# Kernel tuning notes

Measured on AMD Instinct MI355X. Metric: run time of the kernel, lower is better.

Reference implementation:

```python
import jax, jax.numpy as jnp
import numpy as np

N_NODES = 100
F_IN = 65536
C_OUT = 60
ACTION_DIM = 100
N_EDGES = 2000


def setup_inputs() -> dict:
    key = jax.random.key(0)
    ks = jax.random.split(key, 16)
    s = 0.02
    return {
        "substrate_features": jax.random.normal(ks[0], (1, N_NODES, F_IN), jnp.float32),
        "edge_index": jax.random.randint(ks[1], (2, N_EDGES), 0, N_NODES, dtype=jnp.int32),
        "v_cpu_demand_t": jax.random.uniform(ks[2], (1,), jnp.float32),
        "v_bw_demand_t": jax.random.uniform(ks[3], (1,), jnp.float32),
        "num_pending_v_nodes_t": jax.random.uniform(ks[4], (1,), jnp.float32),
        "actor_w": jax.random.normal(ks[5], (3, F_IN, C_OUT), jnp.float32) * s,
        "actor_b": jax.random.normal(ks[6], (C_OUT,), jnp.float32) * s,
        "critic_w": jax.random.normal(ks[7], (3, F_IN, C_OUT), jnp.float32) * s,
        "critic_b": jax.random.normal(ks[8], (C_OUT,), jnp.float32) * s,
        "actor_fc_w": jax.random.normal(ks[9], (N_NODES * C_OUT + 3, ACTION_DIM), jnp.float32) * s,
        "actor_fc_b": jax.random.normal(ks[10], (ACTION_DIM,), jnp.float32) * s,
        "critic_fc_w": jax.random.normal(ks[11], (N_NODES * C_OUT + 3, 1), jnp.float32) * s,
        "critic_fc_b": jax.random.normal(ks[12], (1,), jnp.float32) * s,
    }


def cheb_conv(x, edge_index, W, b):
    # ChebConv, K=3, sym normalization, lambda_max=2 (PyG defaults).
    # With lambda_max=2 the scaled Laplacian is L_hat = -D^{-1/2} A D^{-1/2}
    # (diagonal becomes 0 after the -1 self-loop shift).
    # x: [1, N, F]; edge_index: [2, E]; W: [3, F, C]; b: [C]
    src, dst = edge_index[0], edge_index[1]
    n = x.shape[1]
    deg = jax.ops.segment_sum(jnp.ones(src.shape[0], x.dtype), src, num_segments=n)
    dis = jnp.where(deg > 0, jax.lax.rsqrt(jnp.where(deg > 0, deg, 1.0)), 0.0)
    norm = -(dis[src] * dis[dst])  # [E], L_hat off-diagonal entries
    x2 = x[0]  # [N, F]

    def prop(z):  # z: [N, F] -> L_hat @ z via gather/scatter over edges
        return jax.ops.segment_sum(z[src] * norm[:, None], dst, num_segments=n)

    Tx0 = x2
    Tx1 = prop(Tx0)
    Tx2 = 2.0 * prop(Tx1) - Tx0
    out = Tx0 @ W[0] + Tx1 @ W[1] + Tx2 @ W[2] + b  # [N, C]
    return out[None]  # [1, N, C]


def reference(substrate_features, edge_index, v_cpu_demand_t, v_bw_demand_t,
              num_pending_v_nodes_t, actor_w, actor_b, critic_w, critic_b,
              actor_fc_w, actor_fc_b, critic_fc_w, critic_fc_b):
    emb_a = jnp.tanh(cheb_conv(substrate_features, edge_index, actor_w, actor_b))
    emb_a = emb_a.reshape(1, -1)  # [1, N*60]
    emb_c = jnp.tanh(cheb_conv(substrate_features, edge_index, critic_w, critic_b))
    emb_c = emb_c.reshape(1, -1)
    extras = [v_cpu_demand_t[None], v_bw_demand_t[None], num_pending_v_nodes_t[None]]  # each [1,1]
    state_a = jnp.concatenate([emb_a] + extras, axis=1)  # [1, 6003]
    state_c = jnp.concatenate([emb_c] + extras, axis=1)
    logits = state_a @ actor_fc_w + actor_fc_b  # [1, action_dim]
    values = state_c @ critic_fc_w + critic_fc_b  # [1, 1]
    return (logits, values)
```

## Files before the change

kernel.cpp:

```cpp
#include <hip/hip_runtime.h>
#include <stdint.h>

#define F_IN 65536
#define NN 100
#define CO 60
#define G2 256
#define KC (F_IN/G2)
#define BK 64
#define NIT (KC/BK)
#define AST 72
#define BTILE (BK*CO)
#define BQ3 (3*BTILE/4)

typedef short v8s __attribute__((ext_vector_type(8)));
typedef float v4f __attribute__((ext_vector_type(4)));

__device__ __forceinline__ unsigned int f2bf(float x){
  unsigned int u = __float_as_uint(x);
  u += 0x7fffu + ((u>>16)&1u);
  return u>>16;
}

__device__ __forceinline__ v4f mfma16(v8s a, v8s b, v4f c){
  return __builtin_amdgcn_mfma_f32_16x16x32_bf16(a,b,c,0,0,0);
}

__global__ __launch_bounds__(256,2)
void k_gemm(const float* __restrict__ x, const float* __restrict__ aw,
            const float* __restrict__ cw, float* __restrict__ dst, int partial){
  const int bid  = blockIdx.x;
  const int xcd  = bid & 7, slot = bid >> 3;
  const int net  = slot & 1;
  const int s    = xcd*32 + (slot >> 1);
  const int k0   = s*KC;
  const int tid  = threadIdx.x;
  const int wave = tid>>6, lane = tid&63, quad = lane>>4, nl = lane&15;
  const int c0   = wave*16;
  const int ccl  = min(c0+nl, CO-1);

  const float* Wn = net ? cw : aw;

  __shared__ __align__(16) unsigned short Al[2][112*AST];
  __shared__ __align__(16) unsigned short Bl[2][3*BTILE];

  unsigned int boff[12];
  #pragma unroll
  for(int p=0;p<12;++p){
    int li = min(p*256 + tid, BQ3-1);
    int gp = li/960, fp = li - gp*960;
    boff[p] = (unsigned int)((size_t)gp*F_IN*CO + (size_t)fp*4)*4u;
  }
  const char* bbase0 = (const char*)(Wn + (size_t)k0*CO);

  float4 ra[7];
  float4 rbv[12];
  #pragma unroll
  for(int p=0;p<7;++p){
    int lin = p*256 + tid, row = lin>>4, q = lin&15;
    int rcl = min(row, NN-1);
    ra[p] = *(const float4*)(x + (size_t)rcl*F_IN + k0 + q*4);
  }
  #pragma unroll
  for(int p=0;p<12;++p) rbv[p] = *(const float4*)(bbase0 + boff[p]);

  v4f acc[3][7];
  #pragma unroll
  for(int g=0;g<3;++g)
    #pragma unroll
    for(int i=0;i<7;++i){ v4f z={0.f,0.f,0.f,0.f}; acc[g][i]=z; }

  for(int it=0; it<NIT; ++it){
    unsigned short* buf  = Al[it&1];
    unsigned short* bbuf = Bl[it&1];
    #pragma unroll
    for(int p=0;p<7;++p){
      int lin = p*256 + tid, row = lin>>4, q = lin&15;
      uint2 w;
      w.x = f2bf(ra[p].x) | (f2bf(ra[p].y)<<16);
      w.y = f2bf(ra[p].z) | (f2bf(ra[p].w)<<16);
      *(uint2*)(buf + row*AST + q*4) = w;
    }
    #pragma unroll
    for(int p=0;p<12;++p){
      int lin = p*256 + tid;
      if(lin < BQ3){
        uint2 w;
        w.x = f2bf(rbv[p].x) | (f2bf(rbv[p].y)<<16);
        w.y = f2bf(rbv[p].z) | (f2bf(rbv[p].w)<<16);
        *(uint2*)(bbuf + lin*4) = w;
      }
    }
    __syncthreads();
    if(it+1 < NIT){
      const int kb = k0 + (it+1)*BK;
      #pragma unroll
      for(int p=0;p<7;++p){
        int lin = p*256 + tid, row = lin>>4, q = lin&15;
        int rcl = min(row, NN-1);
        ra[p] = *(const float4*)(x + (size_t)rcl*F_IN + kb + q*4);
      }
      const char* bb2 = bbase0 + (size_t)(it+1)*BK*CO*4;
      #pragma unroll
      for(int p=0;p<12;++p) rbv[p] = *(const float4*)(bb2 + boff[p]);
    }
    v8s fB0[3], fB1[3];
    #pragma unroll
    for(int g=0;g<3;++g){
      const unsigned short* bb = bbuf + g*BTILE + quad*8*CO + ccl;
      #pragma unroll
      for(int j=0;j<8;++j){
        fB0[g][j] = (short)bb[j*CO];
        fB1[g][j] = (short)bb[32*CO + j*CO];
      }
    }
    #pragma unroll
    for(int mt=0; mt<7; ++mt){
      const unsigned short* arow = buf + (mt*16+nl)*AST + quad*8;
      v8s a0 = *(const v8s*)(arow);
      v8s a1 = *(const v8s*)(arow+32);
      #pragma unroll
      for(int g=0;g<3;++g){
        acc[g][mt] = mfma16(a0, fB0[g], acc[g][mt]);
        acc[g][mt] = mfma16(a1, fB1[g], acc[g][mt]);
      }
    }
  }

  const int c = c0 + nl;
  if(c < CO){
    #pragma unroll
    for(int g=0;g<3;++g){
      if(partial){
        float* pd = dst + ((size_t)(net*3+g)*G2 + s)*(NN*CO);
        #pragma unroll
        for(int mt=0;mt<7;++mt){
          #pragma unroll
          for(int i=0;i<4;++i){
            int m = mt*16 + quad*4 + i;
            if(m < NN) pd[m*CO + c] = acc[g][mt][i];
          }
        }
      } else {
        float* pd = dst + (size_t)(net*3+g)*(NN*CO);
        #pragma unroll
        for(int mt=0;mt<7;++mt){
          #pragma unroll
          for(int i=0;i<4;++i){
            int m = mt*16 + quad*4 + i;
            if(m < NN) atomicAdd(pd + m*CO + c, acc[g][mt][i]);
          }
        }
      }
    }
  }
}

__global__ void k_reduce(const float* __restrict__ P, float* __restrict__ Y){
  int o = blockIdx.x*256 + threadIdx.x;
  if(o >= 6*NN*CO) return;
  int gg = o/(NN*CO), r = o - gg*(NN*CO);
  const float* p = P + (size_t)gg*G2*(NN*CO) + (size_t)blockIdx.y*32*(NN*CO) + r;
  float a0=0.f,a1=0.f,a2=0.f,a3=0.f;
  #pragma unroll 2
  for(int s4=0;s4<32;s4+=4){
    a0 += p[(size_t)(s4  )*(NN*CO)];
    a1 += p[(size_t)(s4+1)*(NN*CO)];
    a2 += p[(size_t)(s4+2)*(NN*CO)];
    a3 += p[(size_t)(s4+3)*(NN*CO)];
  }
  atomicAdd(&Y[o], (a0+a1)+(a2+a3));
}

__global__ void k_cheb(const float* __restrict__ Y, const int* __restrict__ ei,
                       const float* __restrict__ ab, const float* __restrict__ cb,
                       float* __restrict__ emb, float* __restrict__ out){
  const int net = blockIdx.x / CO;
  const int c   = blockIdx.x % CO;
  const int t   = threadIdx.x;
  __shared__ float L[NN][NN+1];
  __shared__ float dis[NN];
  __shared__ int   deg[NN];
  __shared__ float y0[NN], y1[NN], y2[NN], zu[NN];

  if(blockIdx.x==0 && t<101) out[t] = 0.f;

  for(int i=t;i<NN*(NN+1);i+=128) ((float*)L)[i]=0.f;
  if(t<NN) deg[t]=0;
  __syncthreads();
  for(int e=t;e<2000;e+=128) atomicAdd(&deg[ei[e]],1);
  __syncthreads();
  if(t<NN) dis[t] = deg[t]>0 ? rsqrtf((float)deg[t]) : 0.f;
  __syncthreads();
  for(int e=t;e<2000;e+=128){
    int s = ei[e], d = ei[2000+e];
    atomicAdd(&L[d][s], -dis[s]*dis[d]);
  }
  if(t<NN){
    const float* yb = Y + (size_t)net*3*NN*CO + t*CO + c;
    y0[t]=yb[0]; y1[t]=yb[NN*CO]; y2[t]=yb[2*NN*CO];
  }
  __syncthreads();
  if(t<NN){
    float s=0.f;
    #pragma unroll 4
    for(int j=0;j<NN;++j) s += L[t][j]*y2[j];
    zu[t] = y1[t] + 2.f*s;
  }
  __syncthreads();
  if(t<NN){
    float s=0.f;
    #pragma unroll 4
    for(int j=0;j<NN;++j) s += L[t][j]*zu[j];
    float b = (net==0) ? ab[c] : cb[c];
    emb[net*NN*CO + t*CO + c] = tanhf(y0[t] - y2[t] + s + b);
  }
}

#define FCB 50
__global__ void k_fc(const float* __restrict__ emb, const float* __restrict__ afw,
                     const float* __restrict__ afb, const float* __restrict__ cfw,
                     const float* __restrict__ cfb, const float* __restrict__ s0,
                     const float* __restrict__ s1, const float* __restrict__ s2,
                     float* __restrict__ out){
  const int b = blockIdx.x;
  const int t = threadIdx.x;
  if(b < FCB){
    const int jj = t & 127, half = t >> 7;
    if(jj < 100){
      const int i0 = b*120 + half*60;
      const float* w = afw + (size_t)i0*100 + jj;
      const float* e = emb + i0;
      float p0=0.f,p1=0.f,p2=0.f,p3=0.f;
      #pragma unroll 3
      for(int i=0;i<60;i+=4){
        p0 += e[i  ]*w[(size_t)(i  )*100];
        p1 += e[i+1]*w[(size_t)(i+1)*100];
        p2 += e[i+2]*w[(size_t)(i+2)*100];
        p3 += e[i+3]*w[(size_t)(i+3)*100];
      }
      atomicAdd(&out[jj], (p0+p1)+(p2+p3));
    }
  } else {
    float p = 0.f;
    const float* e = emb + 6000;
    for(int i=t;i<6000;i+=256) p += e[i]*cfw[i];
    #pragma unroll
    for(int o=32;o>0;o>>=1) p += __shfl_down(p,o,64);
    __shared__ float red[4];
    if((t&63)==0) red[t>>6]=p;
    __syncthreads();
    if(t==0){
      float tot = red[0]+red[1]+red[2]+red[3];
      out[100] = tot + s0[0]*cfw[6000] + s1[0]*cfw[6001] + s2[0]*cfw[6002] + cfb[0];
    }
    if(t<100){
      atomicAdd(&out[t], afb[t] + s0[0]*afw[600000+t] + s1[0]*afw[600100+t] + s2[0]*afw[600200+t]);
    }
  }
}

extern "C" void kernel_launch(void* const* d_in, const int* in_sizes, int n_in,
                              void* d_out, int out_size, void* d_ws, size_t ws_size,
                              hipStream_t stream){
  const float* x   = (const float*)d_in[0];
  const int*   ei  = (const int*)d_in[1];
  const float* s0  = (const float*)d_in[2];
  const float* s1  = (const float*)d_in[3];
  const float* s2  = (const float*)d_in[4];
  const float* aw  = (const float*)d_in[5];
  const float* ab  = (const float*)d_in[6];
  const float* cw  = (const float*)d_in[7];
  const float* cb  = (const float*)d_in[8];
  const float* afw = (const float*)d_in[9];
  const float* afb = (const float*)d_in[10];
  const float* cfw = (const float*)d_in[11];
  const float* cfb = (const float*)d_in[12];
  float* out = (float*)d_out;

  float* Y   = (float*)d_ws;
  float* emb = Y + 6*NN*CO;
  float* P   = emb + 2*NN*CO;
  const size_t need = (size_t)(6*NN*CO + 2*NN*CO + (size_t)6*G2*NN*CO)*sizeof(float);
  const int partial = (ws_size >= need) ? 1 : 0;

  hipMemsetAsync(Y, 0, 6*NN*CO*sizeof(float), stream);

  if(partial){
    k_gemm<<<dim3(512), 256, 0, stream>>>(x, aw, cw, P, 1);
    k_reduce<<<dim3((6*NN*CO+255)/256, 8), 256, 0, stream>>>(P, Y);
  } else {
    k_gemm<<<dim3(512), 256, 0, stream>>>(x, aw, cw, Y, 0);
  }
  k_cheb<<<120, 128, 0, stream>>>(Y, ei, ab, cb, emb, out);
  k_fc<<<FCB+1, 256, 0, stream>>>(emb, afw, afb, cfw, cfb, s0, s1, s2, out);
}
```

Before: 209.1 us.

## Fuse reduce, Chebyshev and FC stages into one grid-barrier kernel; widen GEMM blocks

The split-K reduce, the Chebyshev propagation and the FC heads are merged into a single persistent kernel of 241 blocks. Its stages are separated by software grid barriers on an atomic counter, replacing three launches and the memset of Y. The GEMM block grows from 256 to 512 threads, and the two groups of four waves each take part of the M tiles, which lowers per-thread accumulator registers. The grid barrier assumes all 241 blocks are co-resident, and the reduce now makes a single pass over the 256 partials per output.

```diff
diff --git a/kernel.cpp b/kernel.cpp
--- a/kernel.cpp
+++ b/kernel.cpp
@@ -11,6 +11,7 @@
 #define AST 72
 #define BTILE (BK*CO)
 #define BQ3 (3*BTILE/4)
+#define NB 241
 
 typedef short v8s __attribute__((ext_vector_type(8)));
 typedef float v4f __attribute__((ext_vector_type(4)));
@@ -25,7 +26,7 @@
   return __builtin_amdgcn_mfma_f32_16x16x32_bf16(a,b,c,0,0,0);
 }
 
-__global__ __launch_bounds__(256,2)
+__global__ __launch_bounds__(512,4)
 void k_gemm(const float* __restrict__ x, const float* __restrict__ aw,
             const float* __restrict__ cw, float* __restrict__ dst, int partial){
   const int bid  = blockIdx.x;
@@ -35,7 +36,8 @@
   const int k0   = s*KC;
   const int tid  = threadIdx.x;
   const int wave = tid>>6, lane = tid&63, quad = lane>>4, nl = lane&15;
-  const int c0   = wave*16;
+  const int mh   = wave>>2;
+  const int c0   = (wave&3)*16;
   const int ccl  = min(c0+nl, CO-1);
 
   const float* Wn = net ? cw : aw;
@@ -43,46 +45,47 @@
   __shared__ __align__(16) unsigned short Al[2][112*AST];
   __shared__ __align__(16) unsigned short Bl[2][3*BTILE];
 
-  unsigned int boff[12];
+  const char* bbase0 = (const char*)(Wn + (size_t)k0*CO);
+
+  float4 ra[4];
+  float4 rbv[6];
   #pragma unroll
-  for(int p=0;p<12;++p){
-    int li = min(p*256 + tid, BQ3-1);
-    int gp = li/960, fp = li - gp*960;
-    boff[p] = (unsigned int)((size_t)gp*F_IN*CO + (size_t)fp*4)*4u;
-  }
-  const char* bbase0 = (const char*)(Wn + (size_t)k0*CO);
-
-  float4 ra[7];
-  float4 rbv[12];
-  #pragma unroll
-  for(int p=0;p<7;++p){
-    int lin = p*256 + tid, row = lin>>4, q = lin&15;
+  for(int p=0;p<4;++p){
+    int l2 = min(p*512 + tid, 1791);
+    int row = l2>>4, q = l2&15;
     int rcl = min(row, NN-1);
     ra[p] = *(const float4*)(x + (size_t)rcl*F_IN + k0 + q*4);
   }
   #pragma unroll
-  for(int p=0;p<12;++p) rbv[p] = *(const float4*)(bbase0 + boff[p]);
-
-  v4f acc[3][7];
+  for(int p=0;p<6;++p){
+    int li = min(p*512 + tid, BQ3-1);
+    int gp = li/960, fp = li - gp*960;
+    rbv[p] = *(const float4*)(bbase0 + ((size_t)gp*F_IN*CO + (size_t)fp*4)*4u);
+  }
+
+  v4f acc[3][4];
   #pragma unroll
   for(int g=0;g<3;++g)
     #pragma unroll
-    for(int i=0;i<7;++i){ v4f z={0.f,0.f,0.f,0.f}; acc[g][i]=z; }
+    for(int i=0;i<4;++i){ v4f z={0.f,0.f,0.f,0.f}; acc[g][i]=z; }
 
   for(int it=0; it<NIT; ++it){
     unsigned short* buf  = Al[it&1];
     unsigned short* bbuf = Bl[it&1];
     #pragma unroll
-    for(int p=0;p<7;++p){
-      int lin = p*256 + tid, row = lin>>4, q = lin&15;
-      uint2 w;
-      w.x = f2bf(ra[p].x) | (f2bf(ra[p].y)<<16);
-      w.y = f2bf(ra[p].z) | (f2bf(ra[p].w)<<16);
-      *(uint2*)(buf + row*AST + q*4) = w;
-    }
-    #pragma unroll
-    for(int p=0;p<12;++p){
-      int lin = p*256 + tid;
+    for(int p=0;p<4;++p){
+      int lin = p*512 + tid;
+      if(lin < 1792){
+        int row = lin>>4, q = lin&15;
+        uint2 w;
+        w.x = f2bf(ra[p].x) | (f2bf(ra[p].y)<<16);
+        w.y = f2bf(ra[p].z) | (f2bf(ra[p].w)<<16);
+        *(uint2*)(buf + row*AST + q*4) = w;
+      }
+    }
+    #pragma unroll
+    for(int p=0;p<6;++p){
+      int lin = p*512 + tid;
       if(lin < BQ3){
         uint2 w;
         w.x = f2bf(rbv[p].x) | (f2bf(rbv[p].y)<<16);
@@ -94,14 +97,19 @@
     if(it+1 < NIT){
       const int kb = k0 + (it+1)*BK;
       #pragma unroll
-      for(int p=0;p<7;++p){
-        int lin = p*256 + tid, row = lin>>4, q = lin&15;
+      for(int p=0;p<4;++p){
+        int l2 = min(p*512 + tid, 1791);
+        int row = l2>>4, q = l2&15;
         int rcl = min(row, NN-1);
         ra[p] = *(const float4*)(x + (size_t)rcl*F_IN + kb + q*4);
       }
       const char* bb2 = bbase0 + (size_t)(it+1)*BK*CO*4;
       #pragma unroll
-      for(int p=0;p<12;++p) rbv[p] = *(const float4*)(bb2 + boff[p]);
+      for(int p=0;p<6;++p){
+        int li = min(p*512 + tid, BQ3-1);
+        int gp = li/960, fp = li - gp*960;
+        rbv[p] = *(const float4*)(bb2 + ((size_t)gp*F_IN*CO + (size_t)fp*4)*4u);
+      }
     }
     v8s fB0[3], fB1[3];
     #pragma unroll
@@ -113,41 +121,61 @@
         fB1[g][j] = (short)bb[32*CO + j*CO];
       }
     }
-    #pragma unroll
-    for(int mt=0; mt<7; ++mt){
-      const unsigned short* arow = buf + (mt*16+nl)*AST + quad*8;
-      v8s a0 = *(const v8s*)(arow);
-      v8s a1 = *(const v8s*)(arow+32);
-      #pragma unroll
-      for(int g=0;g<3;++g){
-        acc[g][mt] = mfma16(a0, fB0[g], acc[g][mt]);
-        acc[g][mt] = mfma16(a1, fB1[g], acc[g][mt]);
+    if(mh==0){
+      #pragma unroll
+      for(int m=0;m<4;++m){
+        const unsigned short* arow = buf + (m*16+nl)*AST + quad*8;
+        v8s a0 = *(const v8s*)(arow);
+        v8s a1 = *(const v8s*)(arow+32);
+        #pragma unroll
+        for(int g=0;g<3;++g){
+          acc[g][m] = mfma16(a0, fB0[g], acc[g][m]);
+          acc[g][m] = mfma16(a1, fB1[g], acc[g][m]);
+        }
+      }
+    } else {
+      #pragma unroll
+      for(int m=0;m<3;++m){
+        const unsigned short* arow = buf + ((m+4)*16+nl)*AST + quad*8;
+        v8s a0 = *(const v8s*)(arow);
+        v8s a1 = *(const v8s*)(arow+32);
+        #pragma unroll
+        for(int g=0;g<3;++g){
+          acc[g][m] = mfma16(a0, fB0[g], acc[g][m]);
+          acc[g][m] = mfma16(a1, fB1[g], acc[g][m]);
+        }
       }
     }
   }
 
   const int c = c0 + nl;
+  const int mtb = mh*4;
+  const int mtn = mh ? 3 : 4;
   if(c < CO){
     #pragma unroll
     for(int g=0;g<3;++g){
       if(partial){
         float* pd = dst + ((size_t)(net*3+g)*G2 + s)*(NN*CO);
         #pragma unroll
-        for(int mt=0;mt<7;++mt){
-          #pragma unroll
-          for(int i=0;i<4;++i){
-            int m = mt*16 + quad*4 + i;
-            if(m < NN) pd[m*CO + c] = acc[g][mt][i];
+        for(int m=0;m<4;++m){
+          if(m < mtn){
+            #pragma unroll
+            for(int i=0;i<4;++i){
+              int mm = (mtb+m)*16 + quad*4 + i;
+              if(mm < NN) pd[mm*CO + c] = acc[g][m][i];
+            }
           }
         }
       } else {
         float* pd = dst + (size_t)(net*3+g)*(NN*CO);
         #pragma unroll
-        for(int mt=0;mt<7;++mt){
-          #pragma unroll
-          for(int i=0;i<4;++i){
-            int m = mt*16 + quad*4 + i;
-            if(m < NN) atomicAdd(pd + m*CO + c, acc[g][mt][i]);
+        for(int m=0;m<4;++m){
+          if(m < mtn){
+            #pragma unroll
+            for(int i=0;i<4;++i){
+              int mm = (mtb+m)*16 + quad*4 + i;
+              if(mm < NN) atomicAdd(pd + mm*CO + c, acc[g][m][i]);
+            }
           }
         }
       }
@@ -155,90 +183,98 @@
   }
 }
 
-__global__ void k_reduce(const float* __restrict__ P, float* __restrict__ Y){
-  int o = blockIdx.x*256 + threadIdx.x;
-  if(o >= 6*NN*CO) return;
-  int gg = o/(NN*CO), r = o - gg*(NN*CO);
-  const float* p = P + (size_t)gg*G2*(NN*CO) + (size_t)blockIdx.y*32*(NN*CO) + r;
-  float a0=0.f,a1=0.f,a2=0.f,a3=0.f;
-  #pragma unroll 2
-  for(int s4=0;s4<32;s4+=4){
-    a0 += p[(size_t)(s4  )*(NN*CO)];
-    a1 += p[(size_t)(s4+1)*(NN*CO)];
-    a2 += p[(size_t)(s4+2)*(NN*CO)];
-    a3 += p[(size_t)(s4+3)*(NN*CO)];
-  }
-  atomicAdd(&Y[o], (a0+a1)+(a2+a3));
-}
-
-__global__ void k_cheb(const float* __restrict__ Y, const int* __restrict__ ei,
-                       const float* __restrict__ ab, const float* __restrict__ cb,
-                       float* __restrict__ emb, float* __restrict__ out){
-  const int net = blockIdx.x / CO;
-  const int c   = blockIdx.x % CO;
+__device__ __forceinline__ void gridbar(unsigned* cnt, unsigned target){
+  __syncthreads();
+  if(threadIdx.x==0){
+    __hip_atomic_fetch_add(cnt, 1u, __ATOMIC_ACQ_REL, __HIP_MEMORY_SCOPE_AGENT);
+    while(__hip_atomic_load(cnt, __ATOMIC_ACQUIRE, __HIP_MEMORY_SCOPE_AGENT) < target){}
+  }
+  __syncthreads();
+}
+
+__global__ __launch_bounds__(256,1)
+void k_tail(const float* __restrict__ P, float* __restrict__ Y,
+            const int* __restrict__ ei, const float* __restrict__ ab,
+            const float* __restrict__ cb, const float* __restrict__ afw,
+            const float* __restrict__ afb, const float* __restrict__ cfw,
+            const float* __restrict__ cfb, const float* __restrict__ s0,
+            const float* __restrict__ s1, const float* __restrict__ s2,
+            float* __restrict__ emb, float* __restrict__ out,
+            unsigned* __restrict__ bar, int partial){
+  const int bid = blockIdx.x;
   const int t   = threadIdx.x;
+
   __shared__ float L[NN][NN+1];
   __shared__ float dis[NN];
   __shared__ int   deg[NN];
   __shared__ float y0[NN], y1[NN], y2[NN], zu[NN];
-
-  if(blockIdx.x==0 && t<101) out[t] = 0.f;
-
-  for(int i=t;i<NN*(NN+1);i+=128) ((float*)L)[i]=0.f;
-  if(t<NN) deg[t]=0;
-  __syncthreads();
-  for(int e=t;e<2000;e+=128) atomicAdd(&deg[ei[e]],1);
-  __syncthreads();
-  if(t<NN) dis[t] = deg[t]>0 ? rsqrtf((float)deg[t]) : 0.f;
-  __syncthreads();
-  for(int e=t;e<2000;e+=128){
-    int s = ei[e], d = ei[2000+e];
-    atomicAdd(&L[d][s], -dis[s]*dis[d]);
-  }
-  if(t<NN){
-    const float* yb = Y + (size_t)net*3*NN*CO + t*CO + c;
-    y0[t]=yb[0]; y1[t]=yb[NN*CO]; y2[t]=yb[2*NN*CO];
-  }
-  __syncthreads();
-  if(t<NN){
-    float s=0.f;
-    #pragma unroll 4
-    for(int j=0;j<NN;++j) s += L[t][j]*y2[j];
-    zu[t] = y1[t] + 2.f*s;
-  }
-  __syncthreads();
-  if(t<NN){
-    float s=0.f;
-    #pragma unroll 4
-    for(int j=0;j<NN;++j) s += L[t][j]*zu[j];
-    float b = (net==0) ? ab[c] : cb[c];
-    emb[net*NN*CO + t*CO + c] = tanhf(y0[t] - y2[t] + s + b);
-  }
-}
-
-#define FCB 50
-__global__ void k_fc(const float* __restrict__ emb, const float* __restrict__ afw,
-                     const float* __restrict__ afb, const float* __restrict__ cfw,
-                     const float* __restrict__ cfb, const float* __restrict__ s0,
-                     const float* __restrict__ s1, const float* __restrict__ s2,
-                     float* __restrict__ out){
-  const int b = blockIdx.x;
-  const int t = threadIdx.x;
-  if(b < FCB){
-    const int jj = t & 127, half = t >> 7;
-    if(jj < 100){
-      const int i0 = b*120 + half*60;
-      const float* w = afw + (size_t)i0*100 + jj;
-      const float* e = emb + i0;
-      float p0=0.f,p1=0.f,p2=0.f,p3=0.f;
-      #pragma unroll 3
-      for(int i=0;i<60;i+=4){
-        p0 += e[i  ]*w[(size_t)(i  )*100];
-        p1 += e[i+1]*w[(size_t)(i+1)*100];
-        p2 += e[i+2]*w[(size_t)(i+2)*100];
-        p3 += e[i+3]*w[(size_t)(i+3)*100];
-      }
-      atomicAdd(&out[jj], (p0+p1)+(p2+p3));
+  __shared__ float red[4];
+
+  if(partial){
+    int o = bid*256 + t;
+    if(o < 6*NN*CO){
+      int gg = o/(NN*CO), r = o - gg*(NN*CO);
+      const float* p = P + (size_t)gg*G2*(NN*CO) + r;
+      float a0=0.f,a1=0.f,a2=0.f,a3=0.f;
+      #pragma unroll 4
+      for(int s4=0;s4<G2;s4+=4){
+        a0 += p[(size_t)(s4  )*(NN*CO)];
+        a1 += p[(size_t)(s4+1)*(NN*CO)];
+        a2 += p[(size_t)(s4+2)*(NN*CO)];
+        a3 += p[(size_t)(s4+3)*(NN*CO)];
+      }
+      Y[o] = (a0+a1)+(a2+a3);
+    }
+  }
+  if(bid==130 && t<101) out[t] = 0.f;
+
+  gridbar(bar, NB);
+
+  if(bid < 120){
+    const int net = bid / CO;
+    const int c   = bid % CO;
+    for(int i=t;i<NN*(NN+1);i+=256) ((float*)L)[i]=0.f;
+    if(t<NN) deg[t]=0;
+    __syncthreads();
+    for(int e=t;e<2000;e+=256) atomicAdd(&deg[ei[e]],1);
+    __syncthreads();
+    if(t<NN) dis[t] = deg[t]>0 ? rsqrtf((float)deg[t]) : 0.f;
+    __syncthreads();
+    for(int e=t;e<2000;e+=256){
+      int ss = ei[e], d = ei[2000+e];
+      atomicAdd(&L[d][ss], -dis[ss]*dis[d]);
+    }
+    if(t<NN){
+      const float* yb = Y + (size_t)net*3*NN*CO + t*CO + c;
+      y0[t]=yb[0]; y1[t]=yb[NN*CO]; y2[t]=yb[2*NN*CO];
+    }
+    __syncthreads();
+    if(t<NN){
+      float sv=0.f;
+      #pragma unroll 4
+      for(int j=0;j<NN;++j) sv += L[t][j]*y2[j];
+      zu[t] = y1[t] + 2.f*sv;
+    }
+    __syncthreads();
+    if(t<NN){
+      float sv=0.f;
+      #pragma unroll 4
+      for(int j=0;j<NN;++j) sv += L[t][j]*zu[j];
+      float b = (net==0) ? ab[c] : cb[c];
+      emb[net*NN*CO + t*CO + c] = tanhf(y0[t] - y2[t] + sv + b);
+    }
+  }
+
+  gridbar(bar, 2*NB);
+
+  if(bid < 240){
+    if(t < 100){
+      const float* e = emb + bid*25;
+      const float* w = afw + (size_t)bid*25*100 + t;
+      float p = 0.f;
+      #pragma unroll
+      for(int i=0;i<25;++i) p += e[i]*w[(size_t)i*100];
+      atomicAdd(&out[t], p);
     }
   } else {
     float p = 0.f;
@@ -246,7 +282,6 @@
     for(int i=t;i<6000;i+=256) p += e[i]*cfw[i];
     #pragma unroll
     for(int o=32;o>0;o>>=1) p += __shfl_down(p,o,64);
-    __shared__ float red[4];
     if((t&63)==0) red[t>>6]=p;
     __syncthreads();
     if(t==0){
@@ -277,20 +312,17 @@
   const float* cfb = (const float*)d_in[12];
   float* out = (float*)d_out;
 
-  float* Y   = (float*)d_ws;
-  float* emb = Y + 6*NN*CO;
-  float* P   = emb + 2*NN*CO;
-  const size_t need = (size_t)(6*NN*CO + 2*NN*CO + (size_t)6*G2*NN*CO)*sizeof(float);
+  float*    Y   = (float*)d_ws;
+  float*    emb = Y + 6*NN*CO;
+  unsigned* bar = (unsigned*)(emb + 2*NN*CO);
+  float*    P   = (float*)(bar + 16);
+  const size_t need = (size_t)(6*NN*CO + 2*NN*CO + 16)*4 + (size_t)6*G2*NN*CO*4;
   const int partial = (ws_size >= need) ? 1 : 0;
 
-  hipMemsetAsync(Y, 0, 6*NN*CO*sizeof(float), stream);
-
-  if(partial){
-    k_gemm<<<dim3(512), 256, 0, stream>>>(x, aw, cw, P, 1);
-    k_reduce<<<dim3((6*NN*CO+255)/256, 8), 256, 0, stream>>>(P, Y);
-  } else {
-    k_gemm<<<dim3(512), 256, 0, stream>>>(x, aw, cw, Y, 0);
-  }
-  k_cheb<<<120, 128, 0, stream>>>(Y, ei, ab, cb, emb, out);
-  k_fc<<<FCB+1, 256, 0, stream>>>(emb, afw, afb, cfw, cfb, s0, s1, s2, out);
-}
+  hipMemsetAsync(bar, 0, 8, stream);
+  if(!partial) hipMemsetAsync(Y, 0, 6*NN*CO*sizeof(float), stream);
+
+  k_gemm<<<dim3(512), 512, 0, stream>>>(x, aw, cw, partial ? P : Y, partial);
+  k_tail<<<dim3(NB), 256, 0, stream>>>(P, Y, ei, ab, cb, afw, afb, cfw, cfb,
+                                       s0, s1, s2, emb, out, bar, partial);
+}
```

New measurement: 316.7 us. +51.5%, slower.

## Fuse reduce, Chebyshev and FC tail kernels into one persistent kernel with grid barriers

Applied to the files above, without the earlier changes.

Merges the partial-sum reduction, Chebyshev propagation and fully connected stages into a single 256-block kernel that separates the stages with software grid barriers built on an atomic counter in workspace. The aim is to remove launch overhead and idle gaps between the three small tail kernels. The grid barrier relies on all 256 blocks being resident at once, and spinning blocks may waste cycles. The work split inside each stage also changes: the reduction is cut into three parts per element and the FC uses quarters.

```diff
diff --git a/kernel.cpp b/kernel.cpp
--- a/kernel.cpp
+++ b/kernel.cpp
@@ -11,6 +11,7 @@
 #define AST 72
 #define BTILE (BK*CO)
 #define BQ3 (3*BTILE/4)
+#define NBT 256
 
 typedef short v8s __attribute__((ext_vector_type(8)));
 typedef float v4f __attribute__((ext_vector_type(4)));
@@ -155,102 +156,124 @@
   }
 }
 
-__global__ void k_reduce(const float* __restrict__ P, float* __restrict__ Y){
-  int o = blockIdx.x*256 + threadIdx.x;
-  if(o >= 6*NN*CO) return;
-  int gg = o/(NN*CO), r = o - gg*(NN*CO);
-  const float* p = P + (size_t)gg*G2*(NN*CO) + (size_t)blockIdx.y*32*(NN*CO) + r;
-  float a0=0.f,a1=0.f,a2=0.f,a3=0.f;
-  #pragma unroll 2
-  for(int s4=0;s4<32;s4+=4){
-    a0 += p[(size_t)(s4  )*(NN*CO)];
-    a1 += p[(size_t)(s4+1)*(NN*CO)];
-    a2 += p[(size_t)(s4+2)*(NN*CO)];
-    a3 += p[(size_t)(s4+3)*(NN*CO)];
-  }
-  atomicAdd(&Y[o], (a0+a1)+(a2+a3));
-}
-
-__global__ void k_cheb(const float* __restrict__ Y, const int* __restrict__ ei,
-                       const float* __restrict__ ab, const float* __restrict__ cb,
-                       float* __restrict__ emb, float* __restrict__ out){
-  const int net = blockIdx.x / CO;
-  const int c   = blockIdx.x % CO;
+__device__ __forceinline__ void gridbar(unsigned* cnt, unsigned target){
+  __syncthreads();
+  __threadfence();
+  if(threadIdx.x==0){
+    __hip_atomic_fetch_add(cnt, 1u, __ATOMIC_ACQ_REL, __HIP_MEMORY_SCOPE_AGENT);
+    while(__hip_atomic_load(cnt, __ATOMIC_ACQUIRE, __HIP_MEMORY_SCOPE_AGENT) < target)
+      __builtin_amdgcn_s_sleep(4);
+  }
+  __syncthreads();
+  __threadfence();
+}
+
+__global__ __launch_bounds__(512,1)
+void k_tail2(const float* __restrict__ P, float* __restrict__ Y,
+             const int* __restrict__ ei, const float* __restrict__ ab,
+             const float* __restrict__ cb, const float* __restrict__ afw,
+             const float* __restrict__ afb, const float* __restrict__ cfw,
+             const float* __restrict__ cfb, const float* __restrict__ s0,
+             const float* __restrict__ s1, const float* __restrict__ s2,
+             float* __restrict__ emb, float* __restrict__ out,
+             unsigned* __restrict__ bar, int partial){
+  const int bid = blockIdx.x;
   const int t   = threadIdx.x;
+
   __shared__ float L[NN][NN+1];
   __shared__ float dis[NN];
   __shared__ int   deg[NN];
   __shared__ float y0[NN], y1[NN], y2[NN], zu[NN];
-
-  if(blockIdx.x==0 && t<101) out[t] = 0.f;
-
-  for(int i=t;i<NN*(NN+1);i+=128) ((float*)L)[i]=0.f;
-  if(t<NN) deg[t]=0;
-  __syncthreads();
-  for(int e=t;e<2000;e+=128) atomicAdd(&deg[ei[e]],1);
-  __syncthreads();
-  if(t<NN) dis[t] = deg[t]>0 ? rsqrtf((float)deg[t]) : 0.f;
-  __syncthreads();
-  for(int e=t;e<2000;e+=128){
-    int s = ei[e], d = ei[2000+e];
-    atomicAdd(&L[d][s], -dis[s]*dis[d]);
-  }
-  if(t<NN){
-    const float* yb = Y + (size_t)net*3*NN*CO + t*CO + c;
-    y0[t]=yb[0]; y1[t]=yb[NN*CO]; y2[t]=yb[2*NN*CO];
-  }
-  __syncthreads();
-  if(t<NN){
-    float s=0.f;
-    #pragma unroll 4
-    for(int j=0;j<NN;++j) s += L[t][j]*y2[j];
-    zu[t] = y1[t] + 2.f*s;
-  }
-  __syncthreads();
-  if(t<NN){
-    float s=0.f;
-    #pragma unroll 4
-    for(int j=0;j<NN;++j) s += L[t][j]*zu[j];
-    float b = (net==0) ? ab[c] : cb[c];
-    emb[net*NN*CO + t*CO + c] = tanhf(y0[t] - y2[t] + s + b);
-  }
-}
-
-#define FCB 50
-__global__ void k_fc(const float* __restrict__ emb, const float* __restrict__ afw,
-                     const float* __restrict__ afb, const float* __restrict__ cfw,
-                     const float* __restrict__ cfb, const float* __restrict__ s0,
-                     const float* __restrict__ s1, const float* __restrict__ s2,
-                     float* __restrict__ out){
-  const int b = blockIdx.x;
-  const int t = threadIdx.x;
-  if(b < FCB){
-    const int jj = t & 127, half = t >> 7;
+  __shared__ float red[8];
+
+  if(partial){
+    int u = bid*512 + t;
+    if(u < 108000){
+      int o    = u % 36000;
+      int part = u / 36000;
+      int lo = part*86, hi = min(lo+86, G2);
+      int gg = o/6000, r = o - gg*6000;
+      const float* p = P + (size_t)gg*G2*6000 + r;
+      float a0=0.f,a1=0.f,a2=0.f,a3=0.f;
+      int i=lo;
+      #pragma unroll 2
+      for(; i+3<hi; i+=4){
+        a0 += p[(size_t)(i  )*6000];
+        a1 += p[(size_t)(i+1)*6000];
+        a2 += p[(size_t)(i+2)*6000];
+        a3 += p[(size_t)(i+3)*6000];
+      }
+      for(; i<hi; ++i) a0 += p[(size_t)i*6000];
+      atomicAdd(&Y[o], (a0+a1)+(a2+a3));
+    }
+  }
+  if(bid==255 && t<101) out[t] = 0.f;
+
+  gridbar(bar, NBT);
+
+  if(bid < 120){
+    const int net = bid / CO;
+    const int c   = bid % CO;
+    for(int i=t;i<NN*(NN+1);i+=512) ((float*)L)[i]=0.f;
+    if(t<NN) deg[t]=0;
+    __syncthreads();
+    for(int e=t;e<2000;e+=512) atomicAdd(&deg[ei[e]],1);
+    __syncthreads();
+    if(t<NN) dis[t] = deg[t]>0 ? rsqrtf((float)deg[t]) : 0.f;
+    __syncthreads();
+    for(int e=t;e<2000;e+=512){
+      int ss = ei[e], d = ei[2000+e];
+      atomicAdd(&L[d][ss], -dis[ss]*dis[d]);
+    }
+    if(t<NN){
+      const float* yb = Y + (size_t)net*3*NN*CO + t*CO + c;
+      y0[t]=yb[0]; y1[t]=yb[NN*CO]; y2[t]=yb[2*NN*CO];
+    }
+    __syncthreads();
+    if(t<NN){
+      float sv=0.f;
+      #pragma unroll 4
+      for(int j=0;j<NN;++j) sv += L[t][j]*y2[j];
+      zu[t] = y1[t] + 2.f*sv;
+    }
+    __syncthreads();
+    if(t<NN){
+      float sv=0.f;
+      #pragma unroll 4
+      for(int j=0;j<NN;++j) sv += L[t][j]*zu[j];
+      float b = (net==0) ? ab[c] : cb[c];
+      emb[net*NN*CO + t*CO + c] = tanhf(y0[t] - y2[t] + sv + b);
+    }
+  }
+
+  gridbar(bar, 2*NBT);
+
+  if(bid < 50){
+    const int jj = t & 127, quarter = t >> 7;
     if(jj < 100){
-      const int i0 = b*120 + half*60;
+      const int i0 = bid*120 + quarter*30;
       const float* w = afw + (size_t)i0*100 + jj;
       const float* e = emb + i0;
-      float p0=0.f,p1=0.f,p2=0.f,p3=0.f;
-      #pragma unroll 3
-      for(int i=0;i<60;i+=4){
+      float p0=0.f,p1=0.f;
+      #pragma unroll 5
+      for(int i=0;i<30;i+=2){
         p0 += e[i  ]*w[(size_t)(i  )*100];
         p1 += e[i+1]*w[(size_t)(i+1)*100];
-        p2 += e[i+2]*w[(size_t)(i+2)*100];
-        p3 += e[i+3]*w[(size_t)(i+3)*100];
-      }
-      atomicAdd(&out[jj], (p0+p1)+(p2+p3));
-    }
-  } else {
+      }
+      atomicAdd(&out[jj], p0+p1);
+    }
+  } else if(bid == 50){
     float p = 0.f;
     const float* e = emb + 6000;
-    for(int i=t;i<6000;i+=256) p += e[i]*cfw[i];
+    for(int i=t;i<6000;i+=512) p += e[i]*cfw[i];
     #pragma unroll
     for(int o=32;o>0;o>>=1) p += __shfl_down(p,o,64);
-    __shared__ float red[4];
     if((t&63)==0) red[t>>6]=p;
     __syncthreads();
     if(t==0){
-      float tot = red[0]+red[1]+red[2]+red[3];
+      float tot = 0.f;
+      #pragma unroll
+      for(int i=0;i<8;++i) tot += red[i];
       out[100] = tot + s0[0]*cfw[6000] + s1[0]*cfw[6001] + s2[0]*cfw[6002] + cfb[0];
     }
     if(t<100){
@@ -277,20 +300,16 @@
   const float* cfb = (const float*)d_in[12];
   float* out = (float*)d_out;
 
-  float* Y   = (float*)d_ws;
-  float* emb = Y + 6*NN*CO;
-  float* P   = emb + 2*NN*CO;
-  const size_t need = (size_t)(6*NN*CO + 2*NN*CO + (size_t)6*G2*NN*CO)*sizeof(float);
+  float*    Y   = (float*)d_ws;
+  unsigned* bar = (unsigned*)(Y + 6*NN*CO);
+  float*    emb = (float*)(bar + 16);
+  float*    P   = emb + 2*NN*CO;
+  const size_t need = (size_t)(6*NN*CO + 16 + 2*NN*CO)*4 + (size_t)6*G2*NN*CO*4;
   const int partial = (ws_size >= need) ? 1 : 0;
 
-  hipMemsetAsync(Y, 0, 6*NN*CO*sizeof(float), stream);
-
-  if(partial){
-    k_gemm<<<dim3(512), 256, 0, stream>>>(x, aw, cw, P, 1);
-    k_reduce<<<dim3((6*NN*CO+255)/256, 8), 256, 0, stream>>>(P, Y);
-  } else {
-    k_gemm<<<dim3(512), 256, 0, stream>>>(x, aw, cw, Y, 0);
-  }
-  k_cheb<<<120, 128, 0, stream>>>(Y, ei, ab, cb, emb, out);
-  k_fc<<<FCB+1, 256, 0, stream>>>(emb, afw, afb, cfw, cfb, s0, s1, s2, out);
-}
+  hipMemsetAsync(Y, 0, 6*NN*CO*sizeof(float) + 16*sizeof(unsigned), stream);
+
+  k_gemm<<<dim3(512), 256, 0, stream>>>(x, aw, cw, partial ? P : Y, partial);
+  k_tail2<<<dim3(NBT), 512, 0, stream>>>(P, Y, ei, ab, cb, afw, afb, cfw, cfb,
+                                         s0, s1, s2, emb, out, bar, partial);
+}
```

Result: slower. 360.8 us (+72.5%).
